# Kernel optimization log

Hardware: AMD Instinct MI355X
Metric: run time of the kernel (lower is better)

The kernel has to match this reference:

```python
import jax, jax.numpy as jnp
import numpy as np

B, T, I, H = 65536, 9, 57, 2  # batch, seq_len, input_size, hidden_size


def setup_inputs() -> dict:
    key = jax.random.key(0)
    ks = jax.random.split(key, 7)
    return {
        "x": jax.random.normal(ks[0], (B, T, I), dtype=jnp.float32),
        "W_ih": jax.random.normal(ks[1], (4 * H, I), dtype=jnp.float32) * 0.1,
        "W_hh": jax.random.normal(ks[2], (4 * H, H), dtype=jnp.float32) * 0.1,
        "b_ih": jax.random.normal(ks[3], (4 * H,), dtype=jnp.float32) * 0.1,
        "b_hh": jax.random.normal(ks[4], (4 * H,), dtype=jnp.float32) * 0.1,
        "fc_w": jax.random.normal(ks[5], (1, H), dtype=jnp.float32) * 0.1,
        "fc_b": jax.random.normal(ks[6], (1,), dtype=jnp.float32) * 0.1,
    }


def reference(x, W_ih, W_hh, b_ih, b_hh, fc_w, fc_b):
    # Precompute input contribution to the gates for all timesteps: [B, T, 4H]
    gx = jnp.einsum("bti,gi->btg", x, W_ih) + b_ih + b_hh
    h0 = jnp.zeros((x.shape[0], W_hh.shape[1]), dtype=x.dtype)
    c0 = jnp.zeros_like(h0)

    def step(carry, g_t):
        h, c = carry
        g = g_t + h @ W_hh.T  # [B, 4H]
        i, f, gg, o = jnp.split(g, 4, axis=-1)  # PyTorch gate order: i, f, g, o
        i = jax.nn.sigmoid(i)
        f = jax.nn.sigmoid(f)
        gg = jnp.tanh(gg)
        o = jax.nn.sigmoid(o)
        c = f * c + i * gg
        h = o * jnp.tanh(c)
        return (h, c), None

    (h_T, _), _ = jax.lax.scan(step, (h0, c0), jnp.swapaxes(gx, 0, 1))  # scan over time
    # fc applied to last hidden state: [B, 1]
    return h_T @ fc_w.T + fc_b
```

## Files before the change

kernel.cpp:

```cpp
#include <hip/hip_runtime.h>


#define B_TOTAL 65536
#define T_STEPS 9
#define I_DIM   57
#define BATCH_PER_BLOCK 64
#define ROWS_PER_BLOCK (BATCH_PER_BLOCK * T_STEPS)
#define CHUNK_ROWS 32
#define N_CHUNKS   (ROWS_PER_BLOCK / CHUNK_ROWS)
#define CHUNK_DW   (CHUNK_ROWS * I_DIM)
#define CHUNK_F4   (CHUNK_DW / 4)
#define GX_PAD     9
#define NBLOCKS    (B_TOTAL / BATCH_PER_BLOCK)

__device__ __forceinline__ float fast_tanh(float v) {
    float e = __builtin_amdgcn_exp2f(2.885390082f * v);
    return 1.0f - 2.0f * __builtin_amdgcn_rcpf(e + 1.0f);
}
__device__ __forceinline__ float fast_sig(float v) {
    return 0.5f * fast_tanh(0.5f * v) + 0.5f;
}

#define DPP_ROR_F32(VAR, SRC, CTRL)                                          \
    float VAR = __builtin_bit_cast(float, __builtin_amdgcn_update_dpp(       \
        0, __builtin_bit_cast(int, SRC), (CTRL), 0xF, 0xF, false))

__global__ __launch_bounds__(256, 4)
void lstm_onepass(const float* __restrict__ x,
                  const float* __restrict__ W_ih,
                  const float* __restrict__ W_hh,
                  const float* __restrict__ b_ih,
                  const float* __restrict__ b_hh,
                  const float* __restrict__ fc_w,
                  const float* __restrict__ fc_b,
                  float* __restrict__ out) {
    __shared__ float xs[2][CHUNK_DW];
    __shared__ float gxp[ROWS_PER_BLOCK * GX_PAD];

    const int tid  = threadIdx.x;
    const int wv   = tid >> 6;
    const int cl   = (tid >> 4) & 3;
    const int g    = (tid >> 1) & 7;
    const int p    = tid & 1;

    float wrot[8][8];
#pragma unroll
    for (int d = 0; d < 8; ++d) {
        const int gg = (g + d) & 7;
        const float* wr = W_ih + gg * I_DIM;
#pragma unroll
        for (int k = 0; k < 7; ++k) wrot[d][k] = wr[g + 8 * k];
        wrot[d][7] = (g == 0) ? wr[56] : 0.0f;
    }
    float bsum = b_ih[g] + b_hh[g];
#pragma unroll
    for (int d = 0; d < 8; ++d)
#pragma unroll
        for (int k = 0; k < 8; ++k)
            asm volatile("" : "+v"(wrot[d][k]));

    const float* xblk = x + (size_t)blockIdx.x * (ROWS_PER_BLOCK * I_DIM);

    float4 st0, st1;

#define STAGE_LOAD(C) do {                                                  \
        const float4* xc_ = (const float4*)(xblk + (size_t)(C) * CHUNK_DW); \
        st0 = xc_[tid];                                                     \
        if (tid < CHUNK_F4 - 256) st1 = xc_[256 + tid];                     \
    } while (0)

#define STAGE_WRITE(S) do {                                                 \
        float4* L_ = (float4*)xs[S];                                        \
        L_[tid] = st0;                                                      \
        if (tid < CHUNK_F4 - 256) L_[256 + tid] = st1;                      \
    } while (0)

#define COMPUTE(S, C) do {                                                  \
        const int rl_ = wv * 8 + cl * 2 + p;                                \
        const float* row_ = xs[S] + rl_ * I_DIM;                            \
        float xv_[8];                                                       \
        _Pragma("unroll")                                                   \
        for (int k = 0; k < 7; ++k) xv_[k] = row_[g + 8 * k];               \
        xv_[7] = row_[56];            \
        float acc_[8];                                                      \
        _Pragma("unroll")                                                   \
        for (int d = 0; d < 8; ++d) {                                       \
            float s_ = wrot[d][0] * xv_[0];                                 \
            _Pragma("unroll")                                               \
            for (int k = 1; k < 8; ++k) s_ += wrot[d][k] * xv_[k];          \
            acc_[d] = s_;                                                   \
        }                                                                   \
                       \
        DPP_ROR_F32(r1_, acc_[1], 0x122);                                   \
        DPP_ROR_F32(r2_, acc_[2], 0x124);                                   \
        DPP_ROR_F32(r3_, acc_[3], 0x126);                                   \
        DPP_ROR_F32(r4_, acc_[4], 0x128);                                   \
        DPP_ROR_F32(r5_, acc_[5], 0x12A);                                   \
        DPP_ROR_F32(r6_, acc_[6], 0x12C);                                   \
        DPP_ROR_F32(r7_, acc_[7], 0x12E);                                   \
        float tot_ = ((acc_[0] + r1_) + (r2_ + r3_))                        \
                   + ((r4_ + r5_) + (r6_ + r7_)) + bsum;                    \
        gxp[((C) * CHUNK_ROWS + rl_) * GX_PAD + g] = tot_;                  \
    } while (0)

    STAGE_LOAD(0);
    STAGE_WRITE(0);

#pragma unroll
    for (int cc = 0; cc < N_CHUNKS; ++cc) {
        __syncthreads();
        if (cc + 1 < N_CHUNKS) STAGE_LOAD(cc + 1);
        COMPUTE(cc & 1, cc);
        if (cc + 1 < N_CHUNKS) STAGE_WRITE((cc + 1) & 1);
    }
#undef STAGE_LOAD
#undef STAGE_WRITE
#undef COMPUTE

    __syncthreads();

    if (tid < BATCH_PER_BLOCK) {
        float w0[8], w1[8];
#pragma unroll
        for (int q = 0; q < 8; ++q) {
            w0[q] = W_hh[q * 2];
            w1[q] = W_hh[q * 2 + 1];
        }

        float h0 = 0.f, h1 = 0.f, c0 = 0.f, c1 = 0.f;
        const float* gb = gxp + tid * (T_STEPS * GX_PAD);

#pragma unroll
        for (int t = 0; t < T_STEPS; ++t) {
            const float* pp = gb + t * GX_PAD;
            const float i0 = fast_sig (pp[0] + h0 * w0[0] + h1 * w1[0]);
            const float i1 = fast_sig (pp[1] + h0 * w0[1] + h1 * w1[1]);
            const float f0 = fast_sig (pp[2] + h0 * w0[2] + h1 * w1[2]);
            const float f1 = fast_sig (pp[3] + h0 * w0[3] + h1 * w1[3]);
            const float g0 = fast_tanh(pp[4] + h0 * w0[4] + h1 * w1[4]);
            const float g1 = fast_tanh(pp[5] + h0 * w0[5] + h1 * w1[5]);
            const float o0 = fast_sig (pp[6] + h0 * w0[6] + h1 * w1[6]);
            const float o1 = fast_sig (pp[7] + h0 * w0[7] + h1 * w1[7]);
            c0 = f0 * c0 + i0 * g0;
            c1 = f1 * c1 + i1 * g1;
            h0 = o0 * fast_tanh(c0);
            h1 = o1 * fast_tanh(c1);
        }

        out[blockIdx.x * BATCH_PER_BLOCK + tid] =
            h0 * fc_w[0] + h1 * fc_w[1] + fc_b[0];
    }
}

extern "C" void kernel_launch(void* const* d_in, const int* in_sizes, int n_in,
                              void* d_out, int out_size, void* d_ws, size_t ws_size,
                              hipStream_t stream) {
    const float* x    = (const float*)d_in[0];
    const float* W_ih = (const float*)d_in[1];
    const float* W_hh = (const float*)d_in[2];
    const float* b_ih = (const float*)d_in[3];
    const float* b_hh = (const float*)d_in[4];
    const float* fc_w = (const float*)d_in[5];
    const float* fc_b = (const float*)d_in[6];
    float* out = (float*)d_out;

    lstm_onepass<<<dim3(NBLOCKS), dim3(256), 0, stream>>>(
        x, W_ih, W_hh, b_ih, b_hh, fc_w, fc_b, out);
}
```

Measured before the change: 39.24 us.

## Give each wave a private x staging pipeline and drop block barriers

Each of the four waves now streams its own contiguous 144-row slice of x through a private double-buffered LDS area, using 8-row chunks with a two-deep register prefetch. This removes every __syncthreads from the projection loop and the one before the recurrence. The recurrence also moves from 64 threads in wave 0 to 16 lanes in each of the four waves. The change depends on intra-wave lockstep for LDS visibility between write and read, and it issues more, smaller loads per wave.

```diff
diff --git a/kernel.cpp b/kernel.cpp
--- a/kernel.cpp
+++ b/kernel.cpp
@@ -6,12 +6,13 @@
 #define I_DIM   57
 #define BATCH_PER_BLOCK 64
 #define ROWS_PER_BLOCK (BATCH_PER_BLOCK * T_STEPS)
-#define CHUNK_ROWS 32
-#define N_CHUNKS   (ROWS_PER_BLOCK / CHUNK_ROWS)
-#define CHUNK_DW   (CHUNK_ROWS * I_DIM)
-#define CHUNK_F4   (CHUNK_DW / 4)
-#define GX_PAD     9
-#define NBLOCKS    (B_TOTAL / BATCH_PER_BLOCK)
+#define ROWS_PER_WAVE  (ROWS_PER_BLOCK / 4)
+#define WCHUNK_ROWS 8
+#define N_WCHUNKS   (ROWS_PER_WAVE / WCHUNK_ROWS)
+#define WCHUNK_DW   (WCHUNK_ROWS * I_DIM)
+#define WCHUNK_F4   (WCHUNK_DW / 4)
+#define GX_PAD      9
+#define NBLOCKS     (B_TOTAL / BATCH_PER_BLOCK)
 
 __device__ __forceinline__ float fast_tanh(float v) {
     float e = __builtin_amdgcn_exp2f(2.885390082f * v);
@@ -34,14 +35,16 @@
                   const float* __restrict__ fc_w,
                   const float* __restrict__ fc_b,
                   float* __restrict__ out) {
-    __shared__ float xs[2][CHUNK_DW];
+    __shared__ float xs[4][2][WCHUNK_DW];
     __shared__ float gxp[ROWS_PER_BLOCK * GX_PAD];
 
     const int tid  = threadIdx.x;
     const int wv   = tid >> 6;
-    const int cl   = (tid >> 4) & 3;
-    const int g    = (tid >> 1) & 7;
-    const int p    = tid & 1;
+    const int lane = tid & 63;
+    const int cl   = (lane >> 4) & 3;
+    const int g    = (lane >> 1) & 7;
+    const int p    = lane & 1;
+    const int rin  = cl * 2 + p;
 
     float wrot[8][8];
 #pragma unroll
@@ -59,25 +62,25 @@
         for (int k = 0; k < 8; ++k)
             asm volatile("" : "+v"(wrot[d][k]));
 
-    const float* xblk = x + (size_t)blockIdx.x * (ROWS_PER_BLOCK * I_DIM);
+    const float* xw = x + (size_t)blockIdx.x * (ROWS_PER_BLOCK * I_DIM)
+                        + (size_t)wv * (ROWS_PER_WAVE * I_DIM);
 
     float4 st0, st1;
 
 #define STAGE_LOAD(C) do {                                                  \
-        const float4* xc_ = (const float4*)(xblk + (size_t)(C) * CHUNK_DW); \
-        st0 = xc_[tid];                                                     \
-        if (tid < CHUNK_F4 - 256) st1 = xc_[256 + tid];                     \
+        const float4* xc_ = (const float4*)(xw + (size_t)(C) * WCHUNK_DW);  \
+        st0 = xc_[lane];                                                    \
+        if (lane < WCHUNK_F4 - 64) st1 = xc_[64 + lane];                    \
     } while (0)
 
 #define STAGE_WRITE(S) do {                                                 \
-        float4* L_ = (float4*)xs[S];                                        \
-        L_[tid] = st0;                                                      \
-        if (tid < CHUNK_F4 - 256) L_[256 + tid] = st1;                      \
+        float4* L_ = (float4*)xs[wv][S];                                    \
+        L_[lane] = st0;                                                     \
+        if (lane < WCHUNK_F4 - 64) L_[64 + lane] = st1;                     \
     } while (0)
 
 #define COMPUTE(S, C) do {                                                  \
-        const int rl_ = wv * 8 + cl * 2 + p;                                \
-        const float* row_ = xs[S] + rl_ * I_DIM;                            \
+        const float* row_ = xs[wv][S] + rin * I_DIM;                        \
         float xv_[8];                                                       \
         _Pragma("unroll")                                                   \
         for (int k = 0; k < 7; ++k) xv_[k] = row_[g + 8 * k];               \
@@ -100,26 +103,25 @@
         DPP_ROR_F32(r7_, acc_[7], 0x12E);                                   \
         float tot_ = ((acc_[0] + r1_) + (r2_ + r3_))                        \
                    + ((r4_ + r5_) + (r6_ + r7_)) + bsum;                    \
-        gxp[((C) * CHUNK_ROWS + rl_) * GX_PAD + g] = tot_;                  \
+        gxp[(wv * ROWS_PER_WAVE + (C) * WCHUNK_ROWS + rin) * GX_PAD + g]    \
+            = tot_;                                                         \
     } while (0)
 
     STAGE_LOAD(0);
     STAGE_WRITE(0);
+    STAGE_LOAD(1);
 
 #pragma unroll
-    for (int cc = 0; cc < N_CHUNKS; ++cc) {
-        __syncthreads();
-        if (cc + 1 < N_CHUNKS) STAGE_LOAD(cc + 1);
+    for (int cc = 0; cc < N_WCHUNKS; ++cc) {
         COMPUTE(cc & 1, cc);
-        if (cc + 1 < N_CHUNKS) STAGE_WRITE((cc + 1) & 1);
+        if (cc + 1 < N_WCHUNKS) STAGE_WRITE((cc + 1) & 1);
+        if (cc + 2 < N_WCHUNKS) STAGE_LOAD(cc + 2);
     }
 #undef STAGE_LOAD
 #undef STAGE_WRITE
 #undef COMPUTE
 
-    __syncthreads();
-
-    if (tid < BATCH_PER_BLOCK) {
+    if (lane < 16) {
         float w0[8], w1[8];
 #pragma unroll
         for (int q = 0; q < 8; ++q) {
@@ -127,8 +129,9 @@
             w1[q] = W_hh[q * 2 + 1];
         }
 
+        const int bloc = wv * 16 + lane;
         float h0 = 0.f, h1 = 0.f, c0 = 0.f, c1 = 0.f;
-        const float* gb = gxp + tid * (T_STEPS * GX_PAD);
+        const float* gb = gxp + bloc * (T_STEPS * GX_PAD);
 
 #pragma unroll
         for (int t = 0; t < T_STEPS; ++t) {
@@ -147,7 +150,7 @@
             h1 = o1 * fast_tanh(c1);
         }
 
-        out[blockIdx.x * BATCH_PER_BLOCK + tid] =
+        out[blockIdx.x * BATCH_PER_BLOCK + bloc] =
             h0 * fc_w[0] + h1 * fc_w[1] + fc_b[0];
     }
 }
```

Result: no change. 39.25 us (+0.0%).
